# Kernel optimization log

Measured on AMD Instinct MI355X. Metric: run time of the kernel, lower is better.

Reference implementation:

```python
import jax, jax.numpy as jnp
import numpy as np
import math

HIDDEN_DIM = 256
H2 = HIDDEN_DIM // 2  # 128
FEATURE_TEMPERATURE = math.sqrt(float(HIDDEN_DIM))


def setup_inputs() -> dict:
    key = jax.random.key(0)
    kf, ks, kw1, kb1, kw2, kb2 = jax.random.split(key, 6)
    B, N, D = 2, 1024, 256
    functional_hidden = jax.random.normal(kf, (B, N, D), dtype=jnp.float32)
    structural_hidden = jax.random.normal(ks, (B, N, D), dtype=jnp.float32)
    # relation_mlp params: Linear(1, H2) then Linear(H2, 1)
    bound1 = 1.0  # fan_in = 1
    w1 = jax.random.uniform(kw1, (H2,), jnp.float32, -bound1, bound1)
    b1 = jax.random.uniform(kb1, (H2,), jnp.float32, -bound1, bound1)
    bound2 = 1.0 / math.sqrt(H2)
    w2 = jax.random.uniform(kw2, (H2,), jnp.float32, -bound2, bound2)
    b2 = jax.random.uniform(kb2, (1,), jnp.float32, -bound2, bound2)
    return {"functional_hidden": functional_hidden, "structural_hidden": structural_hidden,
            "w1": w1, "b1": b1, "w2": w2, "b2": b2}


def reference(functional_hidden, structural_hidden, w1, b1, w2, b2):
    # center along feature dim
    fc = functional_hidden - jnp.mean(functional_hidden, axis=-1, keepdims=True)   # [B,N,D]
    sc = structural_hidden - jnp.mean(structural_hidden, axis=-1, keepdims=True)   # [B,N,D]
    # covariance: [B,N,N]
    covariance = jnp.einsum('bnd,bmd->bnm', fc, sc) / FEATURE_TEMPERATURE
    # per-row std norms (un-normalized, as in source: sqrt of sum of squares)
    f_std = jnp.maximum(jnp.sqrt(jnp.sum(fc * fc, axis=-1)), 1e-6)  # [B,N]
    s_std = jnp.maximum(jnp.sqrt(jnp.sum(sc * sc, axis=-1)), 1e-6)  # [B,N]
    denominator = jnp.maximum(f_std[:, :, None] * s_std[:, None, :], 1e-6)  # [B,N,N]
    correlation = jnp.clip(covariance / denominator, -1.0, 1.0)
    assortativity = jnp.exp(correlation)  # [B,N,N]
    # broadcast 2-layer MLP over every pair: Linear(1,H2)-GELU(exact)-Linear(H2,1)
    h = jax.nn.gelu(assortativity[..., None] * w1 + b1, approximate=False)  # [B,N,N,H2]
    out = jnp.einsum('bnmh,h->bnm', h, w2) + b2[0]  # [B,N,N]
    return out
```

## Files before the change

### kernel.cpp

```cpp
#include <hip/hip_runtime.h>
#include <math.h>

#define NB   2
#define NSEQ 1024
#define DD   256
#define LUTN 2048

#define BM 128
#define BN 64
#define MAGIC 0x5CA1AB1Eu

typedef _Float16 f16;
typedef _Float16 f16x8 __attribute__((ext_vector_type(8)));
typedef float f32x4 __attribute__((ext_vector_type(4)));

__device__ __forceinline__ float wrsum(float v) {
#pragma unroll
  for (int off = 32; off > 0; off >>= 1) v += __shfl_xor(v, off, 64);
  return v;
}

__global__ __launch_bounds__(512, 1) void fused_kernel(
    const float* __restrict__ fg, const float* __restrict__ sg,
    const float* __restrict__ w1, const float* __restrict__ b1,
    const float* __restrict__ w2, const float* __restrict__ b2,
    float* __restrict__ lut, unsigned* __restrict__ flags,
    float* __restrict__ out) {
  __shared__ __align__(16) f16 As[2][2][BM * 64];
  __shared__ __align__(16) f16 Bs[2][2][BN * 64];
  __shared__ float lut_s[LUTN + 1];
  __shared__ float mA[BM], rA[BM], mB[BN], rB[BN];

  const int t = threadIdx.x;
  const int lane = t & 63;
  const int w = t >> 6;
  const int wr = w >> 1, wc = w & 1;
  const int la = lane & 15;
  const int kg = lane >> 4;

  const int bid = blockIdx.x;
  const int x = bid & 7, k = bid >> 3;
  const int panel = x + 8 * (k >> 4);
  const int bz  = panel >> 3;
  const int bm0 = (panel & 7) * BM;
  const int bn0 = (k & 15) * BN;

  const float* fb = fg + ((size_t)bz * NSEQ + bm0) * DD;
  const float* sb = sg + ((size_t)bz * NSEQ + bn0) * DD;

  const int ar = t >> 2, ao = t & 3;
  const int br = t >> 3, bc = (t >> 2) & 1, bo = t & 3;

  float4 A0[4], B0[2], A1[4], B1[2];
  float sAa = 0.f, qAa = 0.f, sBa = 0.f, qBa = 0.f;

  auto ld = [&](float4 (&a)[4], float4 (&b)[2], int st) {
    const float* p = &fb[(size_t)ar * DD + st * 64 + ao * 8];
    a[0] = *reinterpret_cast<const float4*>(p);
    a[1] = *reinterpret_cast<const float4*>(p + 4);
    a[2] = *reinterpret_cast<const float4*>(p + 32);
    a[3] = *reinterpret_cast<const float4*>(p + 36);
    const float* q = &sb[(size_t)br * DD + st * 64 + bc * 32 + bo * 8];
    b[0] = *reinterpret_cast<const float4*>(q);
    b[1] = *reinterpret_cast<const float4*>(q + 4);
  };

  auto split8 = [](const float4& u0, const float4& u1, f16x8& hv, f16x8& lv,
                   float& sm, float& sq) {
    const float vals[8] = {u0.x, u0.y, u0.z, u0.w, u1.x, u1.y, u1.z, u1.w};
#pragma unroll
    for (int e = 0; e < 8; ++e) {
      sm += vals[e];
      sq = fmaf(vals[e], vals[e], sq);
      const f16 h = (f16)vals[e];
      hv[e] = h;
      lv[e] = (f16)(vals[e] - (float)h);
    }
  };

  auto cvt_write = [&](float4 (&a)[4], float4 (&b)[2], int pbuf) {
#pragma unroll
    for (int ch = 0; ch < 2; ++ch) {
      f16x8 hv, lv;
      split8(a[2 * ch], a[2 * ch + 1], hv, lv, sAa, qAa);
      f16* base = &As[pbuf][ch][ar * 64];
      *reinterpret_cast<f16x8*>(&base[(ao ^ (ar & 7)) << 3]) = hv;
      *reinterpret_cast<f16x8*>(&base[((4 + ao) ^ (ar & 7)) << 3]) = lv;
    }
    {
      f16x8 hv, lv;
      split8(b[0], b[1], hv, lv, sBa, qBa);
      f16* base = &Bs[pbuf][bc][br * 64];
      *reinterpret_cast<f16x8*>(&base[(bo ^ (br & 7)) << 3]) = hv;
      *reinterpret_cast<f16x8*>(&base[((4 + bo) ^ (br & 7)) << 3]) = lv;
    }
  };

  f32x4 acc[2][2] = {};

  auto do_mfma = [&](int p) {
#pragma unroll
    for (int ks = 0; ks < 2; ++ks) {
      f16x8 ah[2], al[2], bh[2], bl[2];
#pragma unroll
      for (int i = 0; i < 2; ++i) {
        const int r = wr * 32 + 16 * i + la;
        const f16* base = &As[p][ks][r * 64];
        ah[i] = *reinterpret_cast<const f16x8*>(&base[(kg ^ (r & 7)) << 3]);
        al[i] = *reinterpret_cast<const f16x8*>(&base[((4 + kg) ^ (r & 7)) << 3]);
      }
#pragma unroll
      for (int j = 0; j < 2; ++j) {
        const int r = wc * 32 + 16 * j + la;
        const f16* base = &Bs[p][ks][r * 64];
        bh[j] = *reinterpret_cast<const f16x8*>(&base[(kg ^ (r & 7)) << 3]);
        bl[j] = *reinterpret_cast<const f16x8*>(&base[((4 + kg) ^ (r & 7)) << 3]);
      }
#pragma unroll
      for (int i = 0; i < 2; ++i)
#pragma unroll
        for (int j = 0; j < 2; ++j) {
          acc[i][j] = __builtin_amdgcn_mfma_f32_16x16x32_f16(ah[i], bh[j], acc[i][j], 0, 0, 0);
          acc[i][j] = __builtin_amdgcn_mfma_f32_16x16x32_f16(ah[i], bl[j], acc[i][j], 0, 0, 0);
          acc[i][j] = __builtin_amdgcn_mfma_f32_16x16x32_f16(al[i], bh[j], acc[i][j], 0, 0, 0);
        }
    }
  };

  ld(A0, B0, 0);

  {
    const float w1a = w1[lane], b1a = b1[lane], w2a = w2[lane];
    const float w1b = w1[lane + 64], b1b = b1[lane + 64], w2b = w2[lane + 64];
    const float b2v = b2[0];
    int e = bid * 8 + w;
#pragma unroll
    for (int pass = 0; pass < 2; ++pass) {
      if (pass == 1) { if (bid == 0 && w == 0) e = LUTN; else break; }
      const float corr = -1.0f + (float)e * (2.0f / LUTN);
      const float a = expf(corr);
      const float x0 = fmaf(a, w1a, b1a);
      const float x1 = fmaf(a, w1b, b1b);
      const float g0 = 0.5f * x0 * (1.0f + erff(x0 * 0.70710678118654752f));
      const float g1 = 0.5f * x1 * (1.0f + erff(x1 * 0.70710678118654752f));
      float acc2 = fmaf(g1, w2b, g0 * w2a);
      acc2 = wrsum(acc2);
      if (lane == 0)
        __hip_atomic_store(&lut[e], acc2 + b2v, __ATOMIC_RELAXED, __HIP_MEMORY_SCOPE_AGENT);
    }
  }

  cvt_write(A0, B0, 0);
  asm volatile("s_waitcnt vmcnt(0)" ::: "memory");
  __syncthreads();
  if (t == 0)
    __hip_atomic_store(&flags[bid], MAGIC, __ATOMIC_RELAXED, __HIP_MEMORY_SCOPE_AGENT);

  ld(A0, B0, 1);
  ld(A1, B1, 2);

  do_mfma(0);
  cvt_write(A0, B0, 1);
  ld(A0, B0, 3);
  asm volatile("s_waitcnt lgkmcnt(0)" ::: "memory");
  __builtin_amdgcn_s_barrier();
  do_mfma(1);
  cvt_write(A1, B1, 0);
  asm volatile("s_waitcnt lgkmcnt(0)" ::: "memory");
  __builtin_amdgcn_s_barrier();
  do_mfma(0);
  cvt_write(A0, B0, 1);
  if (t < 256)
    while (__hip_atomic_load(&flags[t], __ATOMIC_RELAXED, __HIP_MEMORY_SCOPE_AGENT) != MAGIC) {}
#pragma unroll
  for (int i = t; i <= LUTN; i += 512)
    lut_s[i] = __hip_atomic_load(&lut[i], __ATOMIC_RELAXED, __HIP_MEMORY_SCOPE_AGENT);
  asm volatile("s_waitcnt lgkmcnt(0)" ::: "memory");
  __builtin_amdgcn_s_barrier();
  do_mfma(1);

  auto red4 = [](float v) {
    v += __shfl_xor(v, 1, 64);
    v += __shfl_xor(v, 2, 64);
    return v;
  };
  sAa = red4(sAa); qAa = red4(qAa);
  if ((t & 3) == 0) {
    const float m = sAa * (1.0f / DD);
    mA[ar] = m;
    rA[ar] = 1.0f / fmaxf(sqrtf(fmaxf(qAa - (float)DD * m * m, 0.0f)), 1e-6f);
  }
  sBa = red4(sBa); sBa += __shfl_xor(sBa, 4, 64);
  qBa = red4(qBa); qBa += __shfl_xor(qBa, 4, 64);
  if ((t & 7) == 0) {
    const float m = sBa * (1.0f / DD);
    mB[br] = m;
    rB[br] = 1.0f / fmaxf(sqrtf(fmaxf(qBa - (float)DD * m * m, 0.0f)), 1e-6f);
  }
  __syncthreads();

  float msv[2], rsv[2];
#pragma unroll
  for (int j = 0; j < 2; ++j) {
    const int cl = wc * 32 + 16 * j + la;
    msv[j] = mB[cl];
    rsv[j] = rB[cl];
  }
#pragma unroll
  for (int i = 0; i < 2; ++i) {
#pragma unroll
    for (int rg = 0; rg < 4; ++rg) {
      const int rowl = wr * 32 + 16 * i + 4 * kg + rg;
      const float mfv = mA[rowl];
      const float rfv = rA[rowl];
#pragma unroll
      for (int j = 0; j < 2; ++j) {
        const float cov = acc[i][j][rg] * (1.0f / 16.0f) - 16.0f * mfv * msv[j];
        float corr = fminf(fmaxf(cov * rfv * rsv[j], -1.0f), 1.0f);
        const float tf = (corr + 1.0f) * (float)(LUTN / 2);
        int idx = (int)tf;
        idx = idx > (LUTN - 1) ? (LUTN - 1) : idx;
        const float fr = tf - (float)idx;
        const float lo = lut_s[idx], hi = lut_s[idx + 1];
        out[((size_t)bz * NSEQ + bm0 + rowl) * NSEQ + bn0 + wc * 32 + 16 * j + la]
            = fmaf(fr, hi - lo, lo);
      }
    }
  }
}

extern "C" void kernel_launch(void* const* d_in, const int* in_sizes, int n_in,
                              void* d_out, int out_size, void* d_ws, size_t ws_size,
                              hipStream_t stream) {
  const float* f  = (const float*)d_in[0];
  const float* s  = (const float*)d_in[1];
  const float* w1 = (const float*)d_in[2];
  const float* b1 = (const float*)d_in[3];
  const float* w2 = (const float*)d_in[4];
  const float* b2 = (const float*)d_in[5];
  float* out = (float*)d_out;

  char* ws = (char*)d_ws;
  float* lut = (float*)(ws);
  unsigned* flags = (unsigned*)(ws + 16384);

  fused_kernel<<<256, 512, 0, stream>>>(f, s, w1, b1, w2, b2, lut, flags, out);
}
```

Baseline: 14.91 us.

## Halve row tile to 64 and launch 512 blocks of 256 threads

Shrinks the A tile from 128 to 64 rows so each block runs 4 waves, launching 512 blocks of 256 threads with two blocks per CU. Thread-to-data mapping, LUT slice assignment, flag waits and the register prefetch schedule (now a single register buffer) are reworked to match. The aim is to fill more CUs and improve latency hiding. In exchange, B-tile loads are reused less and the grid-wide spin barrier must wait on twice as many flags, and it assumes all 512 blocks are co-resident.

Result: slower. 16.75 us (+12.3%).

```diff
diff --git a/kernel.cpp b/kernel.cpp
--- a/kernel.cpp
+++ b/kernel.cpp
@@ -6,7 +6,7 @@
 #define DD   256
 #define LUTN 2048
 
-#define BM 128
+#define BM 64
 #define BN 64
 #define MAGIC 0x5CA1AB1Eu
 
@@ -20,7 +20,7 @@
   return v;
 }
 
-__global__ __launch_bounds__(512, 1) void fused_kernel(
+__global__ __launch_bounds__(256, 2) void fused_kernel(
     const float* __restrict__ fg, const float* __restrict__ sg,
     const float* __restrict__ w1, const float* __restrict__ b1,
     const float* __restrict__ w2, const float* __restrict__ b2,
@@ -41,28 +41,29 @@
   const int bid = blockIdx.x;
   const int x = bid & 7, k = bid >> 3;
   const int panel = x + 8 * (k >> 4);
-  const int bz  = panel >> 3;
-  const int bm0 = (panel & 7) * BM;
+  const int bz  = panel >> 4;
+  const int bm0 = (panel & 15) * BM;
   const int bn0 = (k & 15) * BN;
 
   const float* fb = fg + ((size_t)bz * NSEQ + bm0) * DD;
   const float* sb = sg + ((size_t)bz * NSEQ + bn0) * DD;
 
-  const int ar = t >> 2, ao = t & 3;
-  const int br = t >> 3, bc = (t >> 2) & 1, bo = t & 3;
-
-  float4 A0[4], B0[2], A1[4], B1[2];
+  const int sr = t >> 2, so = t & 3;
+
+  float4 Ar[4], Br[4];
   float sAa = 0.f, qAa = 0.f, sBa = 0.f, qBa = 0.f;
 
-  auto ld = [&](float4 (&a)[4], float4 (&b)[2], int st) {
-    const float* p = &fb[(size_t)ar * DD + st * 64 + ao * 8];
-    a[0] = *reinterpret_cast<const float4*>(p);
-    a[1] = *reinterpret_cast<const float4*>(p + 4);
-    a[2] = *reinterpret_cast<const float4*>(p + 32);
-    a[3] = *reinterpret_cast<const float4*>(p + 36);
-    const float* q = &sb[(size_t)br * DD + st * 64 + bc * 32 + bo * 8];
-    b[0] = *reinterpret_cast<const float4*>(q);
-    b[1] = *reinterpret_cast<const float4*>(q + 4);
+  auto ld = [&](int st) {
+    const float* p = &fb[(size_t)sr * DD + st * 64 + so * 8];
+    Ar[0] = *reinterpret_cast<const float4*>(p);
+    Ar[1] = *reinterpret_cast<const float4*>(p + 4);
+    Ar[2] = *reinterpret_cast<const float4*>(p + 32);
+    Ar[3] = *reinterpret_cast<const float4*>(p + 36);
+    const float* q = &sb[(size_t)sr * DD + st * 64 + so * 8];
+    Br[0] = *reinterpret_cast<const float4*>(q);
+    Br[1] = *reinterpret_cast<const float4*>(q + 4);
+    Br[2] = *reinterpret_cast<const float4*>(q + 32);
+    Br[3] = *reinterpret_cast<const float4*>(q + 36);
   };
 
   auto split8 = [](const float4& u0, const float4& u1, f16x8& hv, f16x8& lv,
@@ -78,21 +79,22 @@
     }
   };
 
-  auto cvt_write = [&](float4 (&a)[4], float4 (&b)[2], int pbuf) {
+  auto cvt_write = [&](int pbuf) {
 #pragma unroll
     for (int ch = 0; ch < 2; ++ch) {
       f16x8 hv, lv;
-      split8(a[2 * ch], a[2 * ch + 1], hv, lv, sAa, qAa);
-      f16* base = &As[pbuf][ch][ar * 64];
-      *reinterpret_cast<f16x8*>(&base[(ao ^ (ar & 7)) << 3]) = hv;
-      *reinterpret_cast<f16x8*>(&base[((4 + ao) ^ (ar & 7)) << 3]) = lv;
-    }
-    {
+      split8(Ar[2 * ch], Ar[2 * ch + 1], hv, lv, sAa, qAa);
+      f16* base = &As[pbuf][ch][sr * 64];
+      *reinterpret_cast<f16x8*>(&base[(so ^ (sr & 7)) << 3]) = hv;
+      *reinterpret_cast<f16x8*>(&base[((4 + so) ^ (sr & 7)) << 3]) = lv;
+    }
+#pragma unroll
+    for (int ch = 0; ch < 2; ++ch) {
       f16x8 hv, lv;
-      split8(b[0], b[1], hv, lv, sBa, qBa);
-      f16* base = &Bs[pbuf][bc][br * 64];
-      *reinterpret_cast<f16x8*>(&base[(bo ^ (br & 7)) << 3]) = hv;
-      *reinterpret_cast<f16x8*>(&base[((4 + bo) ^ (br & 7)) << 3]) = lv;
+      split8(Br[2 * ch], Br[2 * ch + 1], hv, lv, sBa, qBa);
+      f16* base = &Bs[pbuf][ch][sr * 64];
+      *reinterpret_cast<f16x8*>(&base[(so ^ (sr & 7)) << 3]) = hv;
+      *reinterpret_cast<f16x8*>(&base[((4 + so) ^ (sr & 7)) << 3]) = lv;
     }
   };
 
@@ -127,13 +129,13 @@
     }
   };
 
-  ld(A0, B0, 0);
+  ld(0);
 
   {
     const float w1a = w1[lane], b1a = b1[lane], w2a = w2[lane];
     const float w1b = w1[lane + 64], b1b = b1[lane + 64], w2b = w2[lane + 64];
     const float b2v = b2[0];
-    int e = bid * 8 + w;
+    int e = bid * 4 + w;
 #pragma unroll
     for (int pass = 0; pass < 2; ++pass) {
       if (pass == 1) { if (bid == 0 && w == 0) e = LUTN; else break; }
@@ -150,30 +152,32 @@
     }
   }
 
-  cvt_write(A0, B0, 0);
+  cvt_write(0);
   asm volatile("s_waitcnt vmcnt(0)" ::: "memory");
   __syncthreads();
   if (t == 0)
     __hip_atomic_store(&flags[bid], MAGIC, __ATOMIC_RELAXED, __HIP_MEMORY_SCOPE_AGENT);
 
-  ld(A0, B0, 1);
-  ld(A1, B1, 2);
+  ld(1);
 
   do_mfma(0);
-  cvt_write(A0, B0, 1);
-  ld(A0, B0, 3);
+  cvt_write(1);
+  ld(2);
   asm volatile("s_waitcnt lgkmcnt(0)" ::: "memory");
   __builtin_amdgcn_s_barrier();
   do_mfma(1);
-  cvt_write(A1, B1, 0);
+  cvt_write(0);
+  ld(3);
   asm volatile("s_waitcnt lgkmcnt(0)" ::: "memory");
   __builtin_amdgcn_s_barrier();
   do_mfma(0);
-  cvt_write(A0, B0, 1);
-  if (t < 256)
+  cvt_write(1);
+  if (t < 256) {
     while (__hip_atomic_load(&flags[t], __ATOMIC_RELAXED, __HIP_MEMORY_SCOPE_AGENT) != MAGIC) {}
-#pragma unroll
-  for (int i = t; i <= LUTN; i += 512)
+    while (__hip_atomic_load(&flags[t + 256], __ATOMIC_RELAXED, __HIP_MEMORY_SCOPE_AGENT) != MAGIC) {}
+  }
+#pragma unroll
+  for (int i = t; i <= LUTN; i += 256)
     lut_s[i] = __hip_atomic_load(&lut[i], __ATOMIC_RELAXED, __HIP_MEMORY_SCOPE_AGENT);
   asm volatile("s_waitcnt lgkmcnt(0)" ::: "memory");
   __builtin_amdgcn_s_barrier();
@@ -185,17 +189,14 @@
     return v;
   };
   sAa = red4(sAa); qAa = red4(qAa);
+  sBa = red4(sBa); qBa = red4(qBa);
   if ((t & 3) == 0) {
-    const float m = sAa * (1.0f / DD);
-    mA[ar] = m;
-    rA[ar] = 1.0f / fmaxf(sqrtf(fmaxf(qAa - (float)DD * m * m, 0.0f)), 1e-6f);
-  }
-  sBa = red4(sBa); sBa += __shfl_xor(sBa, 4, 64);
-  qBa = red4(qBa); qBa += __shfl_xor(qBa, 4, 64);
-  if ((t & 7) == 0) {
-    const float m = sBa * (1.0f / DD);
-    mB[br] = m;
-    rB[br] = 1.0f / fmaxf(sqrtf(fmaxf(qBa - (float)DD * m * m, 0.0f)), 1e-6f);
+    const float ma = sAa * (1.0f / DD);
+    mA[sr] = ma;
+    rA[sr] = 1.0f / fmaxf(sqrtf(fmaxf(qAa - (float)DD * ma * ma, 0.0f)), 1e-6f);
+    const float mb_ = sBa * (1.0f / DD);
+    mB[sr] = mb_;
+    rB[sr] = 1.0f / fmaxf(sqrtf(fmaxf(qBa - (float)DD * mb_ * mb_, 0.0f)), 1e-6f);
   }
   __syncthreads();
 
@@ -244,5 +245,5 @@
   float* lut = (float*)(ws);
   unsigned* flags = (unsigned*)(ws + 16384);
 
-  fused_kernel<<<256, 512, 0, stream>>>(f, s, w1, b1, w2, b2, lut, flags, out);
+  fused_kernel<<<512, 256, 0, stream>>>(f, s, w1, b1, w2, b2, lut, flags, out);
 }
```
